# Performance work log

Measured on AMD Instinct MI355X. Metric: run time of the kernel, lower is better.

## Reference

```python
import jax, jax.numpy as jnp
import numpy as np
import math

B, T, D = 2, 2048, 1024
H = 16
DH = D // H  # 64
ROPE_BASE = 10000.0


def _rope_tables(seq_len, d_head, dtype=jnp.float32):
    inv_freq = 1.0 / (ROPE_BASE ** (jnp.arange(0, d_head, 2, dtype=jnp.float32) / d_head))
    pos = jnp.arange(seq_len, dtype=jnp.float32)
    freqs = jnp.outer(pos, inv_freq)            # [T, DH/2]
    emb = jnp.concatenate([freqs, freqs], -1)   # [T, DH]
    return jnp.cos(emb).astype(dtype), jnp.sin(emb).astype(dtype)


def _rotate_half(x):
    half = x.shape[-1] // 2
    return jnp.concatenate([-x[..., half:], x[..., :half]], axis=-1)


def setup_inputs() -> dict:
    key = jax.random.key(0)
    k1, k2, k3 = jax.random.split(key, 3)
    x = jax.random.normal(k1, (B, T, D), dtype=jnp.float32)
    qkv_w = jax.random.normal(k2, (D, 3 * D), dtype=jnp.float32) * (1.0 / math.sqrt(D))
    out_w = jax.random.normal(k3, (D, D), dtype=jnp.float32) * (1.0 / math.sqrt(D))
    out_b = jnp.zeros((D,), dtype=jnp.float32)
    mask = jnp.tril(jnp.ones((T, T), dtype=bool))[None, None]  # causal [1,1,T,T]
    return {"x": x, "mask": mask, "qkv_w": qkv_w, "out_w": out_w, "out_b": out_b}


def reference(x, mask, qkv_w, out_w, out_b):
    Bv, Tv, Dv = x.shape
    qkv = (x @ qkv_w).reshape(Bv, Tv, 3, H, DH)
    # [B, H, T, DH]
    q = jnp.transpose(qkv[:, :, 0], (0, 2, 1, 3))
    k = jnp.transpose(qkv[:, :, 1], (0, 2, 1, 3))
    v = jnp.transpose(qkv[:, :, 2], (0, 2, 1, 3))
    cos, sin = _rope_tables(Tv, DH, x.dtype)
    cos = cos[None, None]  # [1,1,T,DH]
    sin = sin[None, None]
    q = q * cos + _rotate_half(q) * sin
    k = k * cos + _rotate_half(k) * sin
    scores = jnp.einsum('bhqd,bhkd->bhqk', q, k) / math.sqrt(DH)
    scores = jnp.where(mask, scores, -jnp.inf)
    probs = jax.nn.softmax(scores, axis=-1)  # dropout = identity in eval mode
    out = jnp.einsum('bhqk,bhkd->bhqd', probs, v)
    out = jnp.transpose(out, (0, 2, 1, 3)).reshape(Bv, Tv, Dv)
    return out @ out_w + out_b
```

## Files before the change

kernel.cpp:

```cpp
#include <hip/hip_runtime.h>
#include <math.h>

typedef __attribute__((ext_vector_type(8))) short short8;
typedef __attribute__((ext_vector_type(4))) float f32x4;

static __device__ __forceinline__ unsigned short f2bf(float f) {
  unsigned u = __builtin_bit_cast(unsigned, f);
  u += 0x7fffu + ((u >> 16) & 1u);
  return (unsigned short)(u >> 16);
}
static __device__ __forceinline__ float bf2f(unsigned short h) {
  return __builtin_bit_cast(float, ((unsigned)h) << 16);
}
static __device__ __forceinline__ unsigned pack2bf(float a, float b) {
  return (unsigned)f2bf(a) | ((unsigned)f2bf(b) << 16);
}
static __device__ __forceinline__ unsigned pack2bf_t(float a, float b) {
  return __builtin_amdgcn_perm(__builtin_bit_cast(unsigned, b),
                               __builtin_bit_cast(unsigned, a), 0x07060302u);
}

typedef __attribute__((address_space(3))) unsigned short lds_us;
typedef __attribute__((address_space(1))) const unsigned short gbl_us;

static __device__ __forceinline__ void gld_lds16(const unsigned short* g,
                                                 unsigned short* l) {
  __builtin_amdgcn_global_load_lds((gbl_us*)g, (lds_us*)l, 16, 0, 0);
}

__global__ __launch_bounds__(256) void prep(const float* __restrict__ x,
                                            unsigned short* __restrict__ xb,
                                            const float* __restrict__ qkv_w,
                                            unsigned short* __restrict__ wqkvT,
                                            const float* __restrict__ out_w,
                                            unsigned short* __restrict__ woT) {
  __shared__ unsigned short T[64][68];
  const int blk = blockIdx.x;
  if (blk < 2048) {
    int i = (blk * 256 + threadIdx.x) * 8;
    float4 a = *(const float4*)(x + i);
    float4 b = *(const float4*)(x + i + 4);
    ushort4 u0 = {f2bf(a.x), f2bf(a.y), f2bf(a.z), f2bf(a.w)};
    ushort4 u1 = {f2bf(b.x), f2bf(b.y), f2bf(b.z), f2bf(b.w)};
    *(ushort4*)(xb + i) = u0;
    *(ushort4*)(xb + i + 4) = u1;
    return;
  }
  const float* in;
  unsigned short* out;
  int R, C, bx, by;
  if (blk < 2816) {
    in = qkv_w; out = wqkvT; R = 1024; C = 3072;
    bx = (blk - 2048) % 48; by = (blk - 2048) / 48;
  } else {
    in = out_w; out = woT; R = 1024; C = 1024;
    bx = (blk - 2816) % 16; by = (blk - 2816) / 16;
  }
  const int r0 = by * 64, c0 = bx * 64;
  const int tr = threadIdx.x >> 2;
  const int tc = (threadIdx.x & 3) * 16;
#pragma unroll
  for (int j = 0; j < 4; ++j) {
    float4 v = *(const float4*)(in + (size_t)(r0 + tr) * C + c0 + tc + j * 4);
    ushort4 u = {f2bf(v.x), f2bf(v.y), f2bf(v.z), f2bf(v.w)};
    *(ushort4*)&T[tr][tc + j * 4] = u;
  }
  __syncthreads();
  const int oc = tr;
#pragma unroll
  for (int g = 0; g < 4; ++g) {
    ushort4 u;
    u.x = T[tc + g * 4 + 0][oc];
    u.y = T[tc + g * 4 + 1][oc];
    u.z = T[tc + g * 4 + 2][oc];
    u.w = T[tc + g * 4 + 3][oc];
    *(ushort4*)(out + (size_t)(c0 + oc) * R + r0 + tc + g * 4) = u;
  }
}

__global__ __launch_bounds__(512) void gemm_qkv512(
    const unsigned short* __restrict__ A, const unsigned short* __restrict__ BT,
    unsigned short* __restrict__ qo, unsigned short* __restrict__ ko,
    unsigned short* __restrict__ vo) {
  __shared__ unsigned short As[2][4096];
  __shared__ unsigned short Bs[2][4096];
  const int tid = threadIdx.x;
  const int w = tid >> 6;
  const int lane = tid & 63;
  const int l15 = lane & 15;
  const int quad = lane >> 4;
  const int wm = w >> 2;
  const int wn = w & 3;
  const int m0 = blockIdx.y * 128;
  const int n0 = blockIdx.x * 128;

  f32x4 acc[4][2];
  const f32x4 zero4 = {0.f, 0.f, 0.f, 0.f};
#pragma unroll
  for (int mt = 0; mt < 4; ++mt)
#pragma unroll
    for (int nt = 0; nt < 2; ++nt) acc[mt][nt] = zero4;

  const int srow = tid >> 2;
  const int skch = (tid & 3) ^ ((srow >> 1) & 3);
  const int coff = tid * 8;
  const unsigned short* gA = A + (size_t)(m0 + srow) * 1024 + skch * 8;
  const unsigned short* gB = BT + (size_t)(n0 + srow) * 1024 + skch * 8;

  const int swz = (quad ^ ((l15 >> 1) & 3)) * 8;
  int aoff[4], boff[2];
#pragma unroll
  for (int t = 0; t < 4; ++t)
    aoff[t] = (wm * 64 + t * 16 + l15) * 32 + swz;
#pragma unroll
  for (int t = 0; t < 2; ++t)
    boff[t] = ((wn >> 1) * 64 + (wn & 1) * 16 + t * 32 + l15) * 32 + swz;

  auto issue = [&](int k0, int buf) {
    gld_lds16(gA + k0, &As[buf][coff]);
    gld_lds16(gB + k0, &Bs[buf][coff]);
  };

  issue(0, 0);
  for (int it = 0; it < 32; ++it) {
    const int cur = it & 1;
    __syncthreads();
    if (it + 1 < 32) issue((it + 1) * 32, cur ^ 1);

    short8 af[4], bf[2];
#pragma unroll
    for (int t = 0; t < 4; ++t) af[t] = *(const short8*)(&As[cur][aoff[t]]);
#pragma unroll
    for (int t = 0; t < 2; ++t) bf[t] = *(const short8*)(&Bs[cur][boff[t]]);
#pragma unroll
    for (int mt = 0; mt < 4; ++mt)
#pragma unroll
      for (int nt = 0; nt < 2; ++nt)
        acc[mt][nt] =
            __builtin_amdgcn_mfma_f32_16x16x32_bf16(af[mt], bf[nt], acc[mt][nt], 0, 0, 0);
  }

  const int b = m0 >> 11;
  const int ngrp = n0 + (wn >> 1) * 64;
  const int which = ngrp >> 10;
  const int h = (ngrp & 1023) >> 6;
  const int bh = b * 16 + h;
  if (which < 2) {
    unsigned short* dst = which ? ko : qo;
    const float qs = (which == 0) ? 0.1803368801111f : 1.0f;
    const int p = (wn & 1) * 16 + l15;
    float inv = __builtin_amdgcn_exp2f((float)p * -0.41524101186f) *
                0.15915494309f;
#pragma unroll
    for (int mt = 0; mt < 4; ++mt)
#pragma unroll
      for (int r = 0; r < 4; ++r) {
        int t = (m0 + wm * 64 + mt * 16 + quad * 4 + r) & 2047;
        float rv = __builtin_amdgcn_fractf((float)t * inv);
        float s = __builtin_amdgcn_sinf(rv);
        float c = __builtin_amdgcn_cosf(rv);
        float x0 = acc[mt][0][r], x1 = acc[mt][1][r];
        size_t rowoff = ((size_t)bh * 2048 + t) * 64;
        dst[rowoff + p]      = f2bf((x0 * c - x1 * s) * qs);
        dst[rowoff + p + 32] = f2bf((x1 * c + x0 * s) * qs);
      }
  } else {
#pragma unroll
    for (int mt = 0; mt < 4; ++mt) {
      int t0 = (m0 + wm * 64 + mt * 16 + quad * 4) & 2047;
#pragma unroll
      for (int nt = 0; nt < 2; ++nt) {
        int dh = (wn & 1) * 16 + nt * 32 + l15;
        ushort4 st = {f2bf(acc[mt][nt][0]), f2bf(acc[mt][nt][1]),
                      f2bf(acc[mt][nt][2]), f2bf(acc[mt][nt][3])};
        *(ushort4*)(vo + ((size_t)bh * 64 + dh) * 2048 + t0) = st;
      }
    }
  }
}

__global__ __launch_bounds__(256) void gemm_out(
    const unsigned short* __restrict__ A, const unsigned short* __restrict__ BT,
    const float* __restrict__ bias, float* __restrict__ out) {
  __shared__ unsigned short As[2][4096];
  __shared__ unsigned short Bs[2][2048];
  const int tid = threadIdx.x;
  const int w = tid >> 6;
  const int lane = tid & 63;
  const int l15 = lane & 15;
  const int quad = lane >> 4;
  const int wm = w >> 1, wn = w & 1;
  const int m0 = blockIdx.y * 128;
  const int n0 = blockIdx.x * 64;

  f32x4 acc[4][2];
  const f32x4 zero4 = {0.f, 0.f, 0.f, 0.f};
#pragma unroll
  for (int mt = 0; mt < 4; ++mt)
#pragma unroll
    for (int nt = 0; nt < 2; ++nt) acc[mt][nt] = zero4;

  int aco[2];
  const unsigned short* gA[2];
#pragma unroll
  for (int i = 0; i < 2; ++i) {
    int c = i * 256 + w * 64 + lane;
    int srow = c >> 2;
    int skch = (c & 3) ^ ((srow >> 1) & 3);
    aco[i] = c * 8;
    gA[i] = A + (size_t)(m0 + srow) * 1024 + skch * 8;
  }
  const int bc = w * 64 + lane;
  const int bsrow = bc >> 2;
  const int bskch = (bc & 3) ^ ((bsrow >> 1) & 3);
  const int bco = bc * 8;
  const unsigned short* gB = BT + (size_t)(n0 + bsrow) * 1024 + bskch * 8;

  const int swz = (quad ^ ((l15 >> 1) & 3)) * 8;
  int aoff[4], boff[2];
#pragma unroll
  for (int t = 0; t < 4; ++t) aoff[t] = (wm * 64 + t * 16 + l15) * 32 + swz;
#pragma unroll
  for (int t = 0; t < 2; ++t) boff[t] = (wn * 32 + t * 16 + l15) * 32 + swz;

  auto issue = [&](int k0, int buf) {
#pragma unroll
    for (int i = 0; i < 2; ++i) gld_lds16(gA[i] + k0, &As[buf][aco[i]]);
    gld_lds16(gB + k0, &Bs[buf][bco]);
  };

  issue(0, 0);
  for (int it = 0; it < 32; ++it) {
    const int cur = it & 1;
    __syncthreads();
    if (it + 1 < 32) issue((it + 1) * 32, cur ^ 1);

    short8 af[4], bf[2];
#pragma unroll
    for (int t = 0; t < 4; ++t) af[t] = *(const short8*)(&As[cur][aoff[t]]);
#pragma unroll
    for (int t = 0; t < 2; ++t) bf[t] = *(const short8*)(&Bs[cur][boff[t]]);
#pragma unroll
    for (int mt = 0; mt < 4; ++mt)
#pragma unroll
      for (int nt = 0; nt < 2; ++nt)
        acc[mt][nt] =
            __builtin_amdgcn_mfma_f32_16x16x32_bf16(af[mt], bf[nt], acc[mt][nt], 0, 0, 0);
  }

  const int nbase = n0 + wn * 32;
  float bv[2];
#pragma unroll
  for (int nt = 0; nt < 2; ++nt) bv[nt] = bias[nbase + nt * 16 + l15];
#pragma unroll
  for (int mt = 0; mt < 4; ++mt)
#pragma unroll
    for (int r = 0; r < 4; ++r) {
      int m = m0 + wm * 64 + mt * 16 + quad * 4 + r;
      float* orow = out + (size_t)m * 1024 + nbase + l15;
#pragma unroll
      for (int nt = 0; nt < 2; ++nt) orow[nt * 16] = acc[mt][nt][r] + bv[nt];
    }
}

__global__ __launch_bounds__(256) void attn_mfma(
    const unsigned short* __restrict__ qg, const unsigned short* __restrict__ kg,
    const unsigned short* __restrict__ vtg, unsigned short* __restrict__ og,
    unsigned short* __restrict__ OpA,
    unsigned short* __restrict__ OpB,
    float* __restrict__ Lpart) {
  __shared__ unsigned short Ks[2][4096];
  __shared__ unsigned short Vt[2][4096];
  __shared__ unsigned short Ps[4 * 16 * 64];
  const int bh = blockIdx.x;
  const int slot = blockIdx.y;
  int qb, chunk;
  if (slot < 32) {
    qb = 24 + (slot & 7);
    chunk = slot >> 3;
  } else if (slot < 56) {
    int s = slot - 32;
    qb = 16 + (s & 7);
    chunk = s >> 3;
  } else if (slot < 72) {
    int s = slot - 56;
    qb = 8 + (s & 7);
    chunk = s >> 3;
  } else {
    qb = slot - 72;
    chunk = 0;
  }
  const int n = qb >= 24 ? 4 : (qb >= 16 ? 3 : (qb >= 8 ? 2 : 1));
  const int t0 = chunk * (qb + 1) / n;
  const int t1 = (chunk + 1) * (qb + 1) / n;

  const int tid = threadIdx.x;
  const int w = tid >> 6;
  const int lane = tid & 63;
  const int l15 = lane & 15;
  const int quad = lane >> 4;

  const int gq0 = qb * 64;
  const int qw = w * 16;

  const unsigned short* qrow = qg + ((size_t)bh * 2048 + gq0 + qw + l15) * 64;
  short8 qf0 = *(const short8*)(qrow + quad * 8);
  short8 qf1 = *(const short8*)(qrow + quad * 8 + 32);

  f32x4 acc_o[4];
  const f32x4 zero4 = {0.f, 0.f, 0.f, 0.f};
#pragma unroll
  for (int nt = 0; nt < 4; ++nt) acc_o[nt] = zero4;
  f32x4 acc_l = zero4;
  const short one_bf = (short)0x3F80;
  const short8 ones8 = {one_bf, one_bf, one_bf, one_bf,
                        one_bf, one_bf, one_bf, one_bf};

  const unsigned short* kbase = kg + (size_t)bh * 2048 * 64;
  const unsigned short* vtbase = vtg + (size_t)bh * 64 * 2048;
  unsigned short* pb = &Ps[w * 16 * 64];
  const int prow = l15 * 64;
  const int psw = l15 & 7;

  auto issue = [&](int kb, int buf) {
    const unsigned short* ksrc = kbase + (size_t)(kb * 64) * 64;
    const unsigned short* vsrc = vtbase + kb * 64;
#pragma unroll
    for (int i = 0; i < 2; ++i) {
      int c = (w * 2 + i) * 64 + lane;
      int row = c >> 3, d = c & 7;
      int sc = d ^ (row & 7);
      gld_lds16(ksrc + row * 64 + sc * 8, &Ks[buf][c * 8]);
      gld_lds16(vsrc + (size_t)row * 2048 + sc * 8, &Vt[buf][c * 8]);
    }
  };

  const int kc0 = (quad ^ psw) * 8;
  const int kc1 = kc0 ^ 32;

  issue(t0, 0);
  for (int kb = t0; kb < t1; ++kb) {
    const int cur = (kb - t0) & 1;
    __syncthreads();
    if (kb + 1 < t1) issue(kb + 1, cur ^ 1);

    const unsigned short* kt = Ks[cur];
    const unsigned short* vt = Vt[cur];

    f32x4 s[4];
#pragma unroll
    for (int nt = 0; nt < 4; ++nt) {
      const unsigned short* kr = kt + (nt * 16 + l15) * 64;
      short8 kf0 = *(const short8*)(kr + kc0);
      short8 kf1 = *(const short8*)(kr + kc1);
      f32x4 c = zero4;
      c = __builtin_amdgcn_mfma_f32_16x16x32_bf16(kf0, qf0, c, 0, 0, 0);
      c = __builtin_amdgcn_mfma_f32_16x16x32_bf16(kf1, qf1, c, 0, 0, 0);
      s[nt] = c;
    }

    if (kb == qb) {
#pragma unroll
      for (int nt = 0; nt < 4; ++nt) {
        int klocal = nt * 16 + quad * 4;
        int qlocal = qw + l15;
#pragma unroll
        for (int r = 0; r < 4; ++r)
          if (klocal + r > qlocal) s[nt][r] = -INFINITY;
      }
    }

#pragma unroll
    for (int nt = 0; nt < 4; ++nt) {
      float e0 = __builtin_amdgcn_exp2f(s[nt][0]);
      float e1 = __builtin_amdgcn_exp2f(s[nt][1]);
      float e2 = __builtin_amdgcn_exp2f(s[nt][2]);
      float e3 = __builtin_amdgcn_exp2f(s[nt][3]);
      int base = prow + ((nt * 2 + (quad >> 1)) ^ psw) * 8 + (quad & 1) * 4;
      uint2 pk;
      pk.x = pack2bf_t(e0, e1);
      pk.y = pack2bf_t(e2, e3);
      *(uint2*)&pb[base] = pk;
    }

    short8 pf0 = *(const short8*)&pb[prow + (quad ^ psw) * 8];
    short8 pf1 = *(const short8*)&pb[prow + ((4 + quad) ^ psw) * 8];

    acc_l = __builtin_amdgcn_mfma_f32_16x16x32_bf16(ones8, pf0, acc_l, 0, 0, 0);
    acc_l = __builtin_amdgcn_mfma_f32_16x16x32_bf16(ones8, pf1, acc_l, 0, 0, 0);

#pragma unroll
    for (int nt = 0; nt < 4; ++nt) {
      const unsigned short* vr = vt + (nt * 16 + l15) * 64;
      short8 vf0 = *(const short8*)(vr + kc0);
      short8 vf1 = *(const short8*)(vr + kc1);
      acc_o[nt] = __builtin_amdgcn_mfma_f32_16x16x32_bf16(vf0, pf0, acc_o[nt], 0, 0, 0);
      acc_o[nt] = __builtin_amdgcn_mfma_f32_16x16x32_bf16(vf1, pf1, acc_o[nt], 0, 0, 0);
    }
  }

  float lsum = acc_l[0];

  if (n == 1) {
    float inv_l = 1.0f / lsum;
    const int b = bh >> 4;
    const int h = bh & 15;
    unsigned short* orow =
        og + ((size_t)(b * 2048 + gq0 + qw + l15)) * 1024 + h * 64 + quad * 4;
#pragma unroll
    for (int nt = 0; nt < 4; ++nt) {
      *(unsigned*)(orow + nt * 16) =
          pack2bf(acc_o[nt][0] * inv_l, acc_o[nt][1] * inv_l);
      *(unsigned*)(orow + nt * 16 + 2) =
          pack2bf(acc_o[nt][2] * inv_l, acc_o[nt][3] * inv_l);
    }
  } else {
    const int pidx = (qb < 16) ? (qb - 8) * 2 + chunk
                               : (qb < 24) ? 16 + (qb - 16) * 3 + chunk
                                           : 40 + (qb - 24) * 4 + chunk;
    unsigned short* obase = (pidx < 16)
                                ? OpB + ((size_t)(bh * 16 + pidx)) * 4096
                                : OpA + ((size_t)(bh * 56 + (pidx - 16))) * 4096;
    unsigned short* orow = obase + (qw + l15) * 64 + quad * 4;
#pragma unroll
    for (int nt = 0; nt < 4; ++nt) {
      *(unsigned*)(orow + nt * 16) = pack2bf(acc_o[nt][0], acc_o[nt][1]);
      *(unsigned*)(orow + nt * 16 + 2) = pack2bf(acc_o[nt][2], acc_o[nt][3]);
    }
    if (quad == 0) Lpart[(bh * 72 + pidx) * 64 + qw + l15] = lsum;
  }
}

__global__ __launch_bounds__(256) void attn_combine(
    const unsigned short* __restrict__ OpA, const unsigned short* __restrict__ OpB,
    const float* __restrict__ Lpart, unsigned short* __restrict__ og) {
  int i = blockIdx.x * 256 + threadIdx.x;
  int dh = (i & 15) * 4;
  int q = (i >> 4) & 63;
  int idx = i >> 10;
  int bh = idx / 24;
  int qr = idx - bh * 24;
  int qb = 8 + qr;
  int count = qr < 8 ? 2 : (qr < 16 ? 3 : 4);
  int pstart = qr < 8 ? qr * 2 : (qr < 16 ? 16 + (qr - 8) * 3 : 40 + (qr - 16) * 4);
  float o0 = 0.f, o1 = 0.f, o2 = 0.f, o3 = 0.f, l = 0.f;
  for (int c = 0; c < count; ++c) {
    int pidx = pstart + c;
    const unsigned short* obase =
        (pidx < 16) ? OpB + ((size_t)(bh * 16 + pidx)) * 4096
                    : OpA + ((size_t)(bh * 56 + (pidx - 16))) * 4096;
    ushort4 a = *(const ushort4*)(obase + q * 64 + dh);
    o0 += bf2f(a.x);
    o1 += bf2f(a.y);
    o2 += bf2f(a.z);
    o3 += bf2f(a.w);
    l += Lpart[(bh * 72 + pidx) * 64 + q];
  }
  float inv = 1.0f / l;
  int bb = bh >> 4, h = bh & 15;
  int t = qb * 64 + q;
  unsigned short* orow = og + ((size_t)(bb * 2048 + t)) * 1024 + h * 64 + dh;
  *(unsigned*)(orow) = pack2bf(o0 * inv, o1 * inv);
  *(unsigned*)(orow + 2) = pack2bf(o2 * inv, o3 * inv);
}

extern "C" void kernel_launch(void* const* d_in, const int* in_sizes, int n_in,
                              void* d_out, int out_size, void* d_ws,
                              size_t ws_size, hipStream_t stream) {
  const float* x = (const float*)d_in[0];
  const float* qkv_w = (const float*)d_in[2];
  const float* out_w = (const float*)d_in[3];
  const float* out_b = (const float*)d_in[4];
  float* out = (float*)d_out;

  unsigned short* xb = (unsigned short*)d_ws;
  unsigned short* wqkvT = xb + 4194304;
  unsigned short* woT = wqkvT + 3145728;
  unsigned short* qb16 = woT + 1048576;
  unsigned short* kb16 = qb16 + 4194304;
  unsigned short* vt16 = kb16 + 4194304;
  unsigned short* ab = vt16 + 4194304;
  unsigned short* OpB = ab + 4194304;
  float* Lpart = (float*)(OpB + 4194304);
  unsigned short* OpA = xb;

  prep<<<3072, 256, 0, stream>>>(x, xb, qkv_w, wqkvT, out_w, woT);
  gemm_qkv512<<<dim3(24, 32), 512, 0, stream>>>(xb, wqkvT, qb16, kb16, vt16);
  attn_mfma<<<dim3(32, 80), 256, 0, stream>>>(qb16, kb16, vt16, ab, OpA, OpB,
                                              Lpart);
  attn_combine<<<3072, 256, 0, stream>>>(OpA, OpB, Lpart, ab);
  gemm_out<<<dim3(16, 32), 256, 0, stream>>>(ab, woT, out_b, out);
}
```

Baseline: 191.7 us.

## Halve attention key tile to 32 and raise occupancy hint

Shrinks the per-iteration key/value tile from 64 to 32 keys. This halves the LDS footprint for K, V^T and P, and lets each thread issue one async global-to-LDS load per tensor instead of two. The swizzles for V^T and P are reworked to fit the narrower 32-column layout, and the causal mask now uses global indices. It also adds a min-blocks-per-CU hint of 7 to push more resident blocks per CU. The cost is twice as many loop iterations with a __syncthreads each, and possible register spills from the tighter occupancy bound.

```diff
diff --git a/kernel.cpp b/kernel.cpp
--- a/kernel.cpp
+++ b/kernel.cpp
@@ -263,15 +263,15 @@
     }
 }
 
-__global__ __launch_bounds__(256) void attn_mfma(
+__global__ __launch_bounds__(256, 7) void attn_mfma(
     const unsigned short* __restrict__ qg, const unsigned short* __restrict__ kg,
     const unsigned short* __restrict__ vtg, unsigned short* __restrict__ og,
     unsigned short* __restrict__ OpA,
     unsigned short* __restrict__ OpB,
     float* __restrict__ Lpart) {
-  __shared__ unsigned short Ks[2][4096];
-  __shared__ unsigned short Vt[2][4096];
-  __shared__ unsigned short Ps[4 * 16 * 64];
+  __shared__ unsigned short Ks[2][2048];
+  __shared__ unsigned short Vt[2][2048];
+  __shared__ unsigned short Ps[4 * 16 * 32];
   const int bh = blockIdx.x;
   const int slot = blockIdx.y;
   int qb, chunk;
@@ -291,8 +291,8 @@
     chunk = 0;
   }
   const int n = qb >= 24 ? 4 : (qb >= 16 ? 3 : (qb >= 8 ? 2 : 1));
-  const int t0 = chunk * (qb + 1) / n;
-  const int t1 = (chunk + 1) * (qb + 1) / n;
+  const int t0 = chunk * 2 * (qb + 1) / n;
+  const int t1 = (chunk + 1) * 2 * (qb + 1) / n;
 
   const int tid = threadIdx.x;
   const int w = tid >> 6;
@@ -318,25 +318,27 @@
 
   const unsigned short* kbase = kg + (size_t)bh * 2048 * 64;
   const unsigned short* vtbase = vtg + (size_t)bh * 64 * 2048;
-  unsigned short* pb = &Ps[w * 16 * 64];
-  const int prow = l15 * 64;
-  const int psw = l15 & 7;
+  unsigned short* pb = &Ps[w * 16 * 32];
+  const int prow = l15 * 32;
+  const int ksw = l15 & 7;
+  const int psw = (l15 & 3) ^ ((l15 >> 2) & 3);
+
+  const int c = w * 64 + lane;
+  const int krow = c >> 3;
+  const int ksc = (c & 7) ^ (krow & 7);
+  const int vrow = c >> 2;
+  const int vsc = ((c & 3) ^ (vrow & 3) ^ ((vrow >> 2) & 3)) & 3;
+  const unsigned short* kgsrc = kbase + krow * 64 + ksc * 8;
+  const unsigned short* vgsrc = vtbase + (size_t)vrow * 2048 + vsc * 8;
 
   auto issue = [&](int kb, int buf) {
-    const unsigned short* ksrc = kbase + (size_t)(kb * 64) * 64;
-    const unsigned short* vsrc = vtbase + kb * 64;
-#pragma unroll
-    for (int i = 0; i < 2; ++i) {
-      int c = (w * 2 + i) * 64 + lane;
-      int row = c >> 3, d = c & 7;
-      int sc = d ^ (row & 7);
-      gld_lds16(ksrc + row * 64 + sc * 8, &Ks[buf][c * 8]);
-      gld_lds16(vsrc + (size_t)row * 2048 + sc * 8, &Vt[buf][c * 8]);
-    }
+    gld_lds16(kgsrc + kb * 32 * 64, &Ks[buf][c * 8]);
+    gld_lds16(vgsrc + kb * 32, &Vt[buf][c * 8]);
   };
 
-  const int kc0 = (quad ^ psw) * 8;
+  const int kc0 = ((quad ^ ksw) & 7) * 8;
   const int kc1 = kc0 ^ 32;
+  const int vc = ((quad ^ psw) & 3) * 8;
 
   issue(t0, 0);
   for (int kb = t0; kb < t1; ++kb) {
@@ -347,55 +349,51 @@
     const unsigned short* kt = Ks[cur];
     const unsigned short* vt = Vt[cur];
 
-    f32x4 s[4];
-#pragma unroll
-    for (int nt = 0; nt < 4; ++nt) {
+    f32x4 s[2];
+#pragma unroll
+    for (int nt = 0; nt < 2; ++nt) {
       const unsigned short* kr = kt + (nt * 16 + l15) * 64;
       short8 kf0 = *(const short8*)(kr + kc0);
       short8 kf1 = *(const short8*)(kr + kc1);
-      f32x4 c = zero4;
-      c = __builtin_amdgcn_mfma_f32_16x16x32_bf16(kf0, qf0, c, 0, 0, 0);
-      c = __builtin_amdgcn_mfma_f32_16x16x32_bf16(kf1, qf1, c, 0, 0, 0);
-      s[nt] = c;
-    }
-
-    if (kb == qb) {
-#pragma unroll
-      for (int nt = 0; nt < 4; ++nt) {
-        int klocal = nt * 16 + quad * 4;
-        int qlocal = qw + l15;
+      f32x4 cc = zero4;
+      cc = __builtin_amdgcn_mfma_f32_16x16x32_bf16(kf0, qf0, cc, 0, 0, 0);
+      cc = __builtin_amdgcn_mfma_f32_16x16x32_bf16(kf1, qf1, cc, 0, 0, 0);
+      s[nt] = cc;
+    }
+
+    if ((kb >> 1) == qb) {
+      int gq = gq0 + qw + l15;
+#pragma unroll
+      for (int nt = 0; nt < 2; ++nt) {
+        int gk = kb * 32 + nt * 16 + quad * 4;
 #pragma unroll
         for (int r = 0; r < 4; ++r)
-          if (klocal + r > qlocal) s[nt][r] = -INFINITY;
+          if (gk + r > gq) s[nt][r] = -INFINITY;
       }
     }
 
 #pragma unroll
-    for (int nt = 0; nt < 4; ++nt) {
+    for (int nt = 0; nt < 2; ++nt) {
       float e0 = __builtin_amdgcn_exp2f(s[nt][0]);
       float e1 = __builtin_amdgcn_exp2f(s[nt][1]);
       float e2 = __builtin_amdgcn_exp2f(s[nt][2]);
       float e3 = __builtin_amdgcn_exp2f(s[nt][3]);
-      int base = prow + ((nt * 2 + (quad >> 1)) ^ psw) * 8 + (quad & 1) * 4;
+      int base = prow + (((nt * 2 + (quad >> 1)) ^ psw) & 3) * 8 + (quad & 1) * 4;
       uint2 pk;
       pk.x = pack2bf_t(e0, e1);
       pk.y = pack2bf_t(e2, e3);
       *(uint2*)&pb[base] = pk;
     }
 
-    short8 pf0 = *(const short8*)&pb[prow + (quad ^ psw) * 8];
-    short8 pf1 = *(const short8*)&pb[prow + ((4 + quad) ^ psw) * 8];
-
-    acc_l = __builtin_amdgcn_mfma_f32_16x16x32_bf16(ones8, pf0, acc_l, 0, 0, 0);
-    acc_l = __builtin_amdgcn_mfma_f32_16x16x32_bf16(ones8, pf1, acc_l, 0, 0, 0);
+    short8 pf = *(const short8*)&pb[prow + vc];
+
+    acc_l = __builtin_amdgcn_mfma_f32_16x16x32_bf16(ones8, pf, acc_l, 0, 0, 0);
 
 #pragma unroll
     for (int nt = 0; nt < 4; ++nt) {
-      const unsigned short* vr = vt + (nt * 16 + l15) * 64;
-      short8 vf0 = *(const short8*)(vr + kc0);
-      short8 vf1 = *(const short8*)(vr + kc1);
-      acc_o[nt] = __builtin_amdgcn_mfma_f32_16x16x32_bf16(vf0, pf0, acc_o[nt], 0, 0, 0);
-      acc_o[nt] = __builtin_amdgcn_mfma_f32_16x16x32_bf16(vf1, pf1, acc_o[nt], 0, 0, 0);
+      const unsigned short* vr = vt + (nt * 16 + l15) * 32;
+      short8 vf = *(const short8*)(vr + vc);
+      acc_o[nt] = __builtin_amdgcn_mfma_f32_16x16x32_bf16(vf, pf, acc_o[nt], 0, 0, 0);
     }
   }
 
```

New measurement: 191.7 us. Within noise of the previous version (+0.0%).
